# Kernel optimization log

Hardware: AMD Instinct MI355X
Metric: run time of the kernel (lower is better)

The kernel has to match this reference:

```python
import jax, jax.numpy as jnp
import numpy as np

D = 1024
H = 16
HD = D // H
DFF = 4 * D
B, L = 2, 2048
EPS = 1e-5


def setup_inputs() -> dict:
    key = jax.random.key(0)
    ks = jax.random.split(key, 12)
    s = lambda fan_in: 1.0 / np.sqrt(fan_in)
    inp = {
        "x": jax.random.normal(ks[0], (B, L, D), jnp.float32),
        "mask": jnp.ones((1, 1, L, L), jnp.bool_),
        "ln_g": jnp.ones((D,), jnp.float32),
        "ln_b": jnp.zeros((D,), jnp.float32),
        "qkv_w": jax.random.uniform(ks[1], (3 * D, D), jnp.float32, -s(D), s(D)),
        "qkv_b": jax.random.uniform(ks[2], (3 * D,), jnp.float32, -s(D), s(D)),
        "wo_w": jax.random.uniform(ks[3], (D, D), jnp.float32, -s(D), s(D)),
        "wo_b": jax.random.uniform(ks[4], (D,), jnp.float32, -s(D), s(D)),
        "m0_w": jax.random.uniform(ks[5], (DFF, D), jnp.float32, -s(D), s(D)),
        "m0_b": jax.random.uniform(ks[6], (DFF,), jnp.float32, -s(D), s(D)),
        "m1_w": jax.random.uniform(ks[7], (D, DFF), jnp.float32, -s(DFF), s(DFF)),
        "m1_b": jax.random.uniform(ks[8], (D,), jnp.float32, -s(DFF), s(DFF)),
    }
    return inp


def _layer_norm(x, g, b):
    mu = jnp.mean(x, axis=-1, keepdims=True)
    var = jnp.var(x, axis=-1, keepdims=True)
    return (x - mu) * jax.lax.rsqrt(var + EPS) * g + b


def reference(x, mask, ln_g, ln_b, qkv_w, qkv_b, wo_w, wo_b, m0_w, m0_b, m1_w, m1_b):
    b, l, d = x.shape
    # --- pre-norm self-attention ---
    xn = _layer_norm(x, ln_g, ln_b)
    qkv = xn @ qkv_w.T + qkv_b                       # [B, L, 3D]
    qkv = qkv.reshape(b, l, 3, H, HD).transpose(2, 0, 3, 1, 4)  # [3, B, H, L, HD]
    q, k, v = qkv[0], qkv[1], qkv[2]
    scores = jnp.einsum("bhld,bhmd->bhlm", q, k) / np.sqrt(HD)  # [B, H, L, L]
    scores = jnp.where(mask, scores, -1e9)
    attn = jax.nn.softmax(scores, axis=-1)
    ctx = jnp.einsum("bhlm,bhmd->bhld", attn, v)     # [B, H, L, HD]
    ctx = ctx.transpose(0, 2, 1, 3).reshape(b, l, d)
    x = x + ctx @ wo_w.T + wo_b
    # --- GELU MLP (same shared LayerNorm params) ---
    xn = _layer_norm(x, ln_g, ln_b)
    h = jax.nn.gelu(xn @ m0_w.T + m0_b, approximate=False)
    return x + h @ m1_w.T + m1_b
```

## Files before the change

### kernel.cpp

```cpp
#include <hip/hip_runtime.h>
#include <hip/hip_bf16.h>
#include <math.h>

#define BL 4096
#define DM 1024
#define NH 16
#define HD 64
#define DFF 4096
#define SEQ 2048
#define EPS 1e-5f
#define QSCALE 0.18033688011112042f

typedef __bf16 bf16x8 __attribute__((ext_vector_type(8)));
typedef float f32x4 __attribute__((ext_vector_type(4)));
typedef float f32x16 __attribute__((ext_vector_type(16)));

__device__ __forceinline__ unsigned short f2bf(float f) {
    __hip_bfloat16 h = __float2bfloat16(f);
    return *reinterpret_cast<unsigned short*>(&h);
}

__device__ __forceinline__ unsigned int pack2bf(float p0, float p1) {
    unsigned int u0 = __builtin_bit_cast(unsigned int, p0) + 0x8000u;
    unsigned int u1 = __builtin_bit_cast(unsigned int, p1) + 0x8000u;
    return __builtin_amdgcn_perm(u1, u0, 0x07060302);
}

__device__ __forceinline__ void gload_lds16(const void* g, void* l) {
    __builtin_amdgcn_global_load_lds(
        (const __attribute__((address_space(1))) unsigned int*)g,
        (__attribute__((address_space(3))) unsigned int*)l,
        16, 0, 0);
}

__global__ __launch_bounds__(256)
void f2b4_kernel(const float* __restrict__ s0, const float* __restrict__ s1,
                 const float* __restrict__ s2, const float* __restrict__ s3,
                 unsigned short* __restrict__ d0, unsigned short* __restrict__ d1,
                 unsigned short* __restrict__ d2, unsigned short* __restrict__ d3,
                 int n0, int n1, int n2, int n3) {
    int i = blockIdx.x * 256 + threadIdx.x;
    const float* s; unsigned short* d; int j = i;
    if (j < n0) { s = s0; d = d0; }
    else if ((j -= n0) < n1) { s = s1; d = d1; }
    else if ((j -= n1) < n2) { s = s2; d = d2; }
    else if ((j -= n2) < n3) { s = s3; d = d3; }
    else return;
    float4 v = ((const float4*)s)[j];
    ushort4 o = {f2bf(v.x), f2bf(v.y), f2bf(v.z), f2bf(v.w)};
    ((ushort4*)d)[j] = o;
}

__global__ __launch_bounds__(256)
void ln_kernel(const float* __restrict__ x, const float* __restrict__ g,
               const float* __restrict__ b, unsigned short* __restrict__ o) {
    int row = blockIdx.x;
    int tid = threadIdx.x;
    const float* xr = x + (size_t)row * DM;
    float4 v = *(const float4*)(xr + tid * 4);
    float s  = v.x + v.y + v.z + v.w;
    float ss = v.x*v.x + v.y*v.y + v.z*v.z + v.w*v.w;
    #pragma unroll
    for (int off = 32; off > 0; off >>= 1) {
        s  += __shfl_down(s, off);
        ss += __shfl_down(ss, off);
    }
    __shared__ float ps[4], pss[4];
    __shared__ float sh_mu, sh_rs;
    int wid = tid >> 6, lane = tid & 63;
    if (lane == 0) { ps[wid] = s; pss[wid] = ss; }
    __syncthreads();
    if (tid == 0) {
        float S = ps[0] + ps[1] + ps[2] + ps[3];
        float SS = pss[0] + pss[1] + pss[2] + pss[3];
        float mu = S * (1.0f / DM);
        float var = SS * (1.0f / DM) - mu * mu;
        sh_mu = mu;
        sh_rs = 1.0f / sqrtf(var + EPS);
    }
    __syncthreads();
    float mu = sh_mu, rs = sh_rs;
    float4 gv = *(const float4*)(g + tid * 4);
    float4 bv = *(const float4*)(b + tid * 4);
    ushort4 ov;
    ov.x = f2bf((v.x - mu) * rs * gv.x + bv.x);
    ov.y = f2bf((v.y - mu) * rs * gv.y + bv.y);
    ov.z = f2bf((v.z - mu) * rs * gv.z + bv.z);
    ov.w = f2bf((v.w - mu) * rs * gv.w + bv.w);
    *(ushort4*)(o + (size_t)row * DM + tid * 4) = ov;
}

template <int EPI, int TN, int BK, int KSPLIT, typename OUT_T>
__global__ __launch_bounds__(256)
void gemm_bt_mfma(const unsigned short* __restrict__ A,
                  const unsigned short* __restrict__ B,
                  const float* __restrict__ bias, const float* __restrict__ res,
                  OUT_T* __restrict__ C, int M, int N, int K,
                  unsigned short* __restrict__ vt) {
    constexpr int RPC = 512 / BK;
    constexpr int CA  = 128 / RPC;
    constexpr int CB  = TN / RPC;
    constexpr int FJ  = TN / 32;
    __shared__ unsigned short As[128 * BK];
    __shared__ unsigned short Bs[TN * BK];
    const int tid = threadIdx.x, lane = tid & 63, wave = tid >> 6;

    const int id   = blockIdx.x;
    const int xcd  = id & 7, slot = id >> 3;
    const int R    = (M / 128) >> 3;
    const int by   = xcd * R + (slot % R);
    const int bx   = slot / R;
    const int m0 = by * 128, n0 = bx * TN;
    const int wm = (wave >> 1) * 64, wn = (wave & 1) * (TN / 2);
    const int k0 = blockIdx.y * (K / KSPLIT);

    const int srow = (BK == 32) ? (lane >> 2) : (lane >> 3);
    const int scol = (BK == 32) ? (lane & 3) * 8
                                : ((lane & 7) ^ (srow & 7)) * 8;
    const int fr = lane & 15;
    const int g  = lane >> 4;

    f32x4 acc[4][FJ] = {};

    for (int kt = k0; kt < k0 + K / KSPLIT; kt += BK) {
        __syncthreads();
        #pragma unroll
        for (int ci = 0; ci < (CA + CB) / 4; ci++) {
            const int c = ci * 4 + wave;
            if (c < CA)
                gload_lds16(A + (size_t)(m0 + c * RPC + srow) * K + kt + scol,
                            (char*)As + c * 1024);
            else
                gload_lds16(B + (size_t)(n0 + (c - CA) * RPC + srow) * K + kt + scol,
                            (char*)Bs + (c - CA) * 1024);
        }
        __syncthreads();

        #pragma unroll
        for (int ko = 0; ko < BK / 32; ko++) {
            const int col = (BK == 32) ? (ko * 32 + g * 8)
                                       : (((ko * 4 + g) ^ (fr & 7)) * 8);
            bf16x8 af[4], bfv[FJ];
            #pragma unroll
            for (int i = 0; i < 4; i++)
                af[i] = *(const bf16x8*)(As + (wm + i * 16 + fr) * BK + col);
            #pragma unroll
            for (int j = 0; j < FJ; j++)
                bfv[j] = *(const bf16x8*)(Bs + (wn + j * 16 + fr) * BK + col);
            #pragma unroll
            for (int i = 0; i < 4; i++)
                #pragma unroll
                for (int j = 0; j < FJ; j++)
                    acc[i][j] = __builtin_amdgcn_mfma_f32_16x16x32_bf16(af[i], bfv[j], acc[i][j], 0, 0, 0);
        }
    }

    const int col  = lane & 15;
    const int rowq = (lane >> 4) * 4;
    const bool kz0 = (KSPLIT == 1) || (blockIdx.y == 0);
    float bs[FJ];
    #pragma unroll
    for (int j = 0; j < FJ; j++) bs[j] = bias[n0 + wn + j * 16 + col];
    #pragma unroll
    for (int i = 0; i < 4; i++) {
        #pragma unroll
        for (int r = 0; r < 4; r++) {
            const size_t row = (size_t)(m0 + wm + i * 16 + rowq + r);
            #pragma unroll
            for (int j = 0; j < FJ; j++) {
                const int c = n0 + wn + j * 16 + col;
                const size_t off = row * N + c;
                float v = acc[i][j][r];
                if (EPI != 4) v += bs[j];
                if (EPI == 1) v += res[off];
                if (EPI == 2) {
                    float u = v * (0.7978845608028654f + 0.035677408136300125f * v * v);
                    float e = __builtin_amdgcn_exp2f(u * 2.885390081777927f);
                    float th = 1.0f - 2.0f * __builtin_amdgcn_rcpf(e + 1.0f);
                    v = 0.5f * v * (1.0f + th);
                }
                if (EPI == 3) {
                    if (c < 2048) {
                        float vq = (c < 1024) ? v * QSCALE : v;
                        ((unsigned short*)C)[off] = f2bf(vq);
                    } else {
                        int d = c & 63, hh = (c >> 6) & 15;
                        int bb = (int)(row >> 11), l = (int)(row & 2047);
                        vt[((size_t)((bb * 16 + hh) * 64 + d)) * 2048 + l] = f2bf(v);
                    }
                } else if (EPI == 4) {
                    if (kz0) v += bs[j];
                    unsafeAtomicAdd((float*)C + off, v);
                } else if constexpr (sizeof(OUT_T) == 2) {
                    ((unsigned short*)C)[off] = f2bf(v);
                } else {
                    ((float*)C)[off] = v;
                }
            }
        }
    }
}

__global__ __launch_bounds__(128)
void attn_mfma(const unsigned short* __restrict__ qkv,
               const unsigned short* __restrict__ vt,
               unsigned short* __restrict__ ctx) {
    __shared__ unsigned short Ks[64 * 64];
    __shared__ unsigned short Vts[64 * 64];
    const int bid = blockIdx.x;
    const int xcd = bid & 7, sl = bid >> 3;
    const int qt = sl & 15, pg = sl >> 4;
    const int pair = pg * 8 + xcd;
    const int h = pair & 15, b = pair >> 4;
    const int tid = threadIdx.x, lane = tid & 63, wave = tid >> 6;
    const int hh = lane >> 5, mm = lane & 31;
    const int qw0 = b * 2048 + qt * 128 + wave * 64;

    bf16x8 qf[2][4];
    #pragma unroll
    for (int g2 = 0; g2 < 2; g2++) {
        const unsigned short* qb = qkv + (size_t)(qw0 + g2 * 32 + mm) * 3072 + h * 64 + hh * 8;
        #pragma unroll
        for (int s = 0; s < 4; s++) qf[g2][s] = *(const bf16x8*)(qb + s * 16);
    }

    const int skey = lane >> 3;
    const int sgr  = (lane & 7) ^ (skey & 7);
    const unsigned short* kbase = qkv + ((size_t)(b * 2048) + skey) * 3072 + 1024 + h * 64 + sgr * 8;
    const unsigned short* vbase = vt + ((size_t)((b * 16 + h) * 64) + skey) * 2048 + sgr * 8;

    float l_lane[2] = {};
    f32x16 o_acc[2][2] = {};

    for (int kt = 0; kt < SEQ; kt += 64) {
        __syncthreads();
        #pragma unroll
        for (int rep = 0; rep < 4; rep++) {
            int c = rep * 2 + wave;
            gload_lds16(kbase + (size_t)(kt + c * 8) * 3072, (char*)Ks + c * 1024);
            gload_lds16(vbase + (size_t)(c * 8) * 2048 + kt, (char*)Vts + c * 1024);
        }
        __syncthreads();

        unsigned int pk[2][2][8];
        #pragma unroll
        for (int g2 = 0; g2 < 2; g2++) {
            f32x16 sT[2] = {};
            #pragma unroll
            for (int t = 0; t < 2; t++)
                #pragma unroll
                for (int s = 0; s < 4; s++) {
                    bf16x8 kf = *(const bf16x8*)(Ks + (t * 32 + mm) * 64 + ((s * 2 + hh) ^ (mm & 7)) * 8);
                    sT[t] = __builtin_amdgcn_mfma_f32_32x32x16_bf16(kf, qf[g2][s], sT[t], 0, 0, 0);
                }
            #pragma unroll
            for (int t = 0; t < 2; t++)
                #pragma unroll
                for (int e = 0; e < 8; e++) {
                    float p0 = __builtin_amdgcn_exp2f(sT[t][2 * e]);
                    float p1 = __builtin_amdgcn_exp2f(sT[t][2 * e + 1]);
                    l_lane[g2] += p0 + p1;
                    pk[g2][t][e] = pack2bf(p0, p1);
                }
        }

        #pragma unroll
        for (int w = 0; w < 4; w++) {
            const int t = w >> 1, eb = (w & 1) * 4;
            bf16x8 af[2];
            #pragma unroll
            for (int g2 = 0; g2 < 2; g2++) {
                unsigned int sx = hh ? pk[g2][t][eb + 0] : pk[g2][t][eb + 2];
                unsigned int sy = hh ? pk[g2][t][eb + 1] : pk[g2][t][eb + 3];
                unsigned int rx = (unsigned int)__shfl_xor((int)sx, 32);
                unsigned int ry = (unsigned int)__shfl_xor((int)sy, 32);
                union { unsigned int u[4]; bf16x8 v; } a;
                a.u[0] = hh ? rx : pk[g2][t][eb + 0];
                a.u[1] = hh ? ry : pk[g2][t][eb + 1];
                a.u[2] = hh ? pk[g2][t][eb + 2] : rx;
                a.u[3] = hh ? pk[g2][t][eb + 3] : ry;
                af[g2] = a.v;
            }
            #pragma unroll
            for (int dt = 0; dt < 2; dt++) {
                bf16x8 vf = *(const bf16x8*)(Vts + (dt * 32 + mm) * 64 + ((w * 2 + hh) ^ (mm & 7)) * 8);
                #pragma unroll
                for (int g2 = 0; g2 < 2; g2++)
                    o_acc[g2][dt] = __builtin_amdgcn_mfma_f32_32x32x16_bf16(af[g2], vf, o_acc[g2][dt], 0, 0, 0);
            }
        }
    }

    #pragma unroll
    for (int g2 = 0; g2 < 2; g2++) {
        float inv_own = 1.0f / (l_lane[g2] + __shfl_xor(l_lane[g2], 32));
        #pragma unroll
        for (int r = 0; r < 16; r++) {
            const int rowq = (r & 3) + 8 * (r >> 2) + 4 * hh;
            float inv = __shfl(inv_own, rowq);
            size_t base = (size_t)(qw0 + g2 * 32 + rowq) * 1024 + h * 64 + mm;
            ctx[base]      = f2bf(o_acc[g2][0][r] * inv);
            ctx[base + 32] = f2bf(o_acc[g2][1][r] * inv);
        }
    }
}

extern "C" void kernel_launch(void* const* d_in, const int* in_sizes, int n_in,
                              void* d_out, int out_size, void* d_ws, size_t ws_size,
                              hipStream_t stream) {
    const float* x     = (const float*)d_in[0];
    const float* ln_g  = (const float*)d_in[2];
    const float* ln_b  = (const float*)d_in[3];
    const float* qkv_w = (const float*)d_in[4];
    const float* qkv_b = (const float*)d_in[5];
    const float* wo_w  = (const float*)d_in[6];
    const float* wo_b  = (const float*)d_in[7];
    const float* m0_w  = (const float*)d_in[8];
    const float* m0_b  = (const float*)d_in[9];
    const float* m1_w  = (const float*)d_in[10];
    const float* m1_b  = (const float*)d_in[11];
    float* out = (float*)d_out;

    char* ws = (char*)d_ws;
    unsigned short* xn_bf  = (unsigned short*)(ws);
    unsigned short* qkv_bf = (unsigned short*)(ws + (size_t)8  * 1024 * 1024);
    unsigned short* vt_bf  = (unsigned short*)(ws + (size_t)32 * 1024 * 1024);
    unsigned short* ctx_bf = (unsigned short*)(ws + (size_t)40 * 1024 * 1024);
    unsigned short* h_bf   = (unsigned short*)(ws + (size_t)48 * 1024 * 1024);
    unsigned short* qkvw_b = (unsigned short*)(ws + (size_t)80 * 1024 * 1024);
    unsigned short* wow_b  = (unsigned short*)(ws + (size_t)86 * 1024 * 1024);
    unsigned short* m0w_b  = (unsigned short*)(ws + (size_t)88 * 1024 * 1024);
    unsigned short* m1w_b  = (unsigned short*)(ws + (size_t)96 * 1024 * 1024);

    {
        int n0 = 3 * DM * DM / 4, n1 = DM * DM / 4, n2 = DFF * DM / 4, n3 = DM * DFF / 4;
        int tot = n0 + n1 + n2 + n3;
        f2b4_kernel<<<(tot + 255) / 256, 256, 0, stream>>>(
            qkv_w, wo_w, m0_w, m1_w, qkvw_b, wow_b, m0w_b, m1w_b, n0, n1, n2, n3);
    }

    ln_kernel<<<BL, 256, 0, stream>>>(x, ln_g, ln_b, xn_bf);
    gemm_bt_mfma<3, 128, 32, 1, unsigned short><<<(3072 / 128) * (BL / 128), 256, 0, stream>>>(
        xn_bf, qkvw_b, qkv_b, nullptr, qkv_bf, BL, 3072, DM, vt_bf);
    attn_mfma<<<2 * NH * (SEQ / 128), 128, 0, stream>>>(qkv_bf, vt_bf, ctx_bf);
    gemm_bt_mfma<1, 64, 32, 1, float><<<(DM / 64) * (BL / 128), 256, 0, stream>>>(
        ctx_bf, wow_b, wo_b, x, out, BL, DM, DM, nullptr);
    ln_kernel<<<BL, 256, 0, stream>>>(out, ln_g, ln_b, xn_bf);
    gemm_bt_mfma<2, 128, 32, 1, unsigned short><<<(DFF / 128) * (BL / 128), 256, 0, stream>>>(
        xn_bf, m0w_b, m0_b, nullptr, h_bf, BL, DFF, DM, nullptr);
    gemm_bt_mfma<4, 64, 64, 2, float><<<dim3((DM / 64) * (BL / 128), 2), 256, 0, stream>>>(
        h_bf, m1w_b, m1_b, nullptr, out, BL, DM, DFF, nullptr);
}
```

Baseline: 372.5 us.

## Split attention KV range across two blocks and merge partials in a combine kernel

Each attention block now handles half of the key/value sequence, selected by a second grid dimension, which doubles the number of blocks. Every block writes its unnormalized fp32 output and row sums to workspace. A new kernel adds the two partials, divides by the summed normalizer, and writes bf16 context. This targets low occupancy in the attention grid, at the cost of extra fp32 workspace traffic and one more launch.

```diff
diff --git a/kernel.cpp b/kernel.cpp
--- a/kernel.cpp
+++ b/kernel.cpp
@@ -204,7 +204,7 @@
 __global__ __launch_bounds__(128)
 void attn_mfma(const unsigned short* __restrict__ qkv,
                const unsigned short* __restrict__ vt,
-               unsigned short* __restrict__ ctx) {
+               float* __restrict__ o_ws, float* __restrict__ l_ws) {
     __shared__ unsigned short Ks[64 * 64];
     __shared__ unsigned short Vts[64 * 64];
     const int bid = blockIdx.x;
@@ -215,6 +215,9 @@
     const int tid = threadIdx.x, lane = tid & 63, wave = tid >> 6;
     const int hh = lane >> 5, mm = lane & 31;
     const int qw0 = b * 2048 + qt * 128 + wave * 64;
+    const int kv0 = blockIdx.y * (SEQ / 2);
+    o_ws += (size_t)blockIdx.y * BL * DM;
+    l_ws += (size_t)blockIdx.y * BL * NH;
 
     bf16x8 qf[2][4];
     #pragma unroll
@@ -232,7 +235,7 @@
     float l_lane[2] = {};
     f32x16 o_acc[2][2] = {};
 
-    for (int kt = 0; kt < SEQ; kt += 64) {
+    for (int kt = kv0; kt < kv0 + SEQ / 2; kt += 64) {
         __syncthreads();
         #pragma unroll
         for (int rep = 0; rep < 4; rep++) {
@@ -293,16 +296,32 @@
 
     #pragma unroll
     for (int g2 = 0; g2 < 2; g2++) {
-        float inv_own = 1.0f / (l_lane[g2] + __shfl_xor(l_lane[g2], 32));
+        float l_full = l_lane[g2] + __shfl_xor(l_lane[g2], 32);
+        if (hh == 0)
+            l_ws[(size_t)(qw0 + g2 * 32 + mm) * NH + h] = l_full;
         #pragma unroll
         for (int r = 0; r < 16; r++) {
             const int rowq = (r & 3) + 8 * (r >> 2) + 4 * hh;
-            float inv = __shfl(inv_own, rowq);
             size_t base = (size_t)(qw0 + g2 * 32 + rowq) * 1024 + h * 64 + mm;
-            ctx[base]      = f2bf(o_acc[g2][0][r] * inv);
-            ctx[base + 32] = f2bf(o_acc[g2][1][r] * inv);
-        }
-    }
+            o_ws[base]      = o_acc[g2][0][r];
+            o_ws[base + 32] = o_acc[g2][1][r];
+        }
+    }
+}
+
+__global__ __launch_bounds__(256)
+void attn_combine(const float* __restrict__ o0, const float* __restrict__ o1,
+                  const float* __restrict__ l0, const float* __restrict__ l1,
+                  unsigned short* __restrict__ ctx) {
+    const int row = blockIdx.x, tid = threadIdx.x;
+    const int h = tid >> 4;
+    const size_t off = (size_t)row * DM + tid * 4;
+    float4 a = *(const float4*)(o0 + off);
+    float4 b = *(const float4*)(o1 + off);
+    float inv = 1.0f / (l0[row * NH + h] + l1[row * NH + h]);
+    ushort4 o = {f2bf((a.x + b.x) * inv), f2bf((a.y + b.y) * inv),
+                 f2bf((a.z + b.z) * inv), f2bf((a.w + b.w) * inv)};
+    *(ushort4*)(ctx + off) = o;
 }
 
 extern "C" void kernel_launch(void* const* d_in, const int* in_sizes, int n_in,
@@ -331,6 +350,8 @@
     unsigned short* wow_b  = (unsigned short*)(ws + (size_t)86 * 1024 * 1024);
     unsigned short* m0w_b  = (unsigned short*)(ws + (size_t)88 * 1024 * 1024);
     unsigned short* m1w_b  = (unsigned short*)(ws + (size_t)96 * 1024 * 1024);
+    float*          o_ws   = (float*)(ws + (size_t)104 * 1024 * 1024);
+    float*          l_ws   = (float*)(ws + (size_t)136 * 1024 * 1024);
 
     {
         int n0 = 3 * DM * DM / 4, n1 = DM * DM / 4, n2 = DFF * DM / 4, n3 = DM * DFF / 4;
@@ -342,7 +363,10 @@
     ln_kernel<<<BL, 256, 0, stream>>>(x, ln_g, ln_b, xn_bf);
     gemm_bt_mfma<3, 128, 32, 1, unsigned short><<<(3072 / 128) * (BL / 128), 256, 0, stream>>>(
         xn_bf, qkvw_b, qkv_b, nullptr, qkv_bf, BL, 3072, DM, vt_bf);
-    attn_mfma<<<2 * NH * (SEQ / 128), 128, 0, stream>>>(qkv_bf, vt_bf, ctx_bf);
+    attn_mfma<<<dim3(2 * NH * (SEQ / 128), 2), 128, 0, stream>>>(
+        qkv_bf, vt_bf, o_ws, l_ws);
+    attn_combine<<<BL, 256, 0, stream>>>(o_ws, o_ws + (size_t)BL * DM,
+                                         l_ws, l_ws + (size_t)BL * NH, ctx_bf);
     gemm_bt_mfma<1, 64, 32, 1, float><<<(DM / 64) * (BL / 128), 256, 0, stream>>>(
         ctx_bf, wow_b, wo_b, x, out, BL, DM, DM, nullptr);
     ln_kernel<<<BL, 256, 0, stream>>>(out, ln_g, ln_b, xn_bf);
```

After: 381.3 us. +2.3%, slower.
